# Optimization experiments

Measured on AMD Instinct MI355X. Metric: run time of the kernel, lower is better.

The kernel has to match this reference:

```python
import jax, jax.numpy as jnp
import numpy as np

DIM = 1024
HEADS = 16
HEAD_DIM = DIM // HEADS


def setup_inputs() -> dict:
    key = jax.random.key(0)
    ks = jax.random.split(key, 10)
    B, N, M = 4, 2048, 2048
    s = 1.0 / np.sqrt(DIM)
    return {
        "x": jax.random.normal(ks[0], (B, N, DIM), jnp.float32),
        "context": jax.random.normal(ks[1], (B, M, DIM), jnp.float32),
        "Wq": jax.random.normal(ks[2], (DIM, DIM), jnp.float32) * s,
        "bq": jnp.zeros((DIM,), jnp.float32),
        "Wk": jax.random.normal(ks[3], (DIM, DIM), jnp.float32) * s,
        "bk": jnp.zeros((DIM,), jnp.float32),
        "Wv": jax.random.normal(ks[4], (DIM, DIM), jnp.float32) * s,
        "bv": jnp.zeros((DIM,), jnp.float32),
        "Wo": jax.random.normal(ks[5], (DIM, DIM), jnp.float32) * s,
        "bo": jnp.zeros((DIM,), jnp.float32),
    }


def reference(x, context, Wq, bq, Wk, bk, Wv, bv, Wo, bo):
    B, N, C = x.shape
    M = context.shape[1]
    scale = HEAD_DIM ** (-0.5)
    # projections + split heads: [B, H, L, D]
    q = (x @ Wq.T + bq).reshape(B, N, HEADS, HEAD_DIM).transpose(0, 2, 1, 3)
    k = (context @ Wk.T + bk).reshape(B, M, HEADS, HEAD_DIM).transpose(0, 2, 1, 3)
    v = (context @ Wv.T + bv).reshape(B, M, HEADS, HEAD_DIM).transpose(0, 2, 1, 3)
    attn = jax.nn.softmax(jnp.einsum('bhnd,bhmd->bhnm', q, k) * scale, axis=-1)
    out = jnp.einsum('bhnm,bhmd->bhnd', attn, v)  # [B, H, N, D]
    out = out.transpose(0, 2, 1, 3).reshape(B, N, C)
    return out @ Wo.T + bo
```

## Files before the change

kernel.cpp:

```cpp
#include <hip/hip_runtime.h>
#include <hip/hip_bf16.h>
#include <stdint.h>


#define HEADS 16
#define HD 64
#define NSEQ 2048
#define DIMSZ 1024

typedef __bf16 bf16x8_t __attribute__((ext_vector_type(8)));
typedef float f32x4_t __attribute__((ext_vector_type(4)));
typedef short s16x4 __attribute__((ext_vector_type(4)));
typedef unsigned short u16;
typedef unsigned int u32;

__device__ __forceinline__ u16 f2bf(float f) {
    union { float f; u32 i; } x; x.f = f;
    u32 r = x.i + 0x7FFF + ((x.i >> 16) & 1);
    return (u16)(r >> 16);
}
__device__ __forceinline__ u32 pk2(float a, float b) {
    __hip_bfloat162 h = __float22bfloat162_rn(float2{a, b});
    union { __hip_bfloat162 h2; u32 u; } c; c.h2 = h; return c.u;
}

#if defined(__has_builtin)
#if __has_builtin(__builtin_amdgcn_exp2f)
#define EXP2(x) __builtin_amdgcn_exp2f(x)
#endif
#endif
#ifndef EXP2
#define EXP2(x) exp2f(x)
#endif

__device__ __forceinline__ void pl32swap(u32& a, u32& b) {
    asm("v_permlane32_swap_b32 %0, %1" : "+v"(a), "+v"(b));
}
__device__ __forceinline__ void pl16swap(u32& a, u32& b) {
    asm("v_permlane16_swap_b32 %0, %1" : "+v"(a), "+v"(b));
}

#define GLDS(g, l) __builtin_amdgcn_global_load_lds( \
    (const __attribute__((address_space(1))) void*)(g), \
    (__attribute__((address_space(3))) void*)(l), 16, 0, 0)

__global__ __launch_bounds__(256)
void cvt_all(const float* __restrict__ x, const float* __restrict__ ctx,
             const float* __restrict__ wq, const float* __restrict__ wk,
             const float* __restrict__ wv, const float* __restrict__ wo,
             u16* __restrict__ xb, u16* __restrict__ ctxb,
             u16* __restrict__ wqb, u16* __restrict__ wkb,
             u16* __restrict__ wvb, u16* __restrict__ wob)
{
    long g = (long)blockIdx.x * 256 + threadIdx.x;
    const float* in; u16* out; long off;
    if (g < 1048576L)      { in = x;   out = xb;   off = g; }
    else if (g < 2097152L) { in = ctx; out = ctxb; off = g - 1048576L; }
    else if (g < 2228224L) { in = wq;  out = wqb;  off = g - 2097152L; }
    else if (g < 2359296L) { in = wk;  out = wkb;  off = g - 2228224L; }
    else if (g < 2490368L) { in = wv;  out = wvb;  off = g - 2359296L; }
    else                   { in = wo;  out = wob;  off = g - 2490368L; }
    long i = off * 8;
    float4 a = *(const float4*)(in + i);
    float4 b = *(const float4*)(in + i + 4);
    union { uint4 v; u16 h[8]; } u;
    u.h[0] = f2bf(a.x); u.h[1] = f2bf(a.y); u.h[2] = f2bf(a.z); u.h[3] = f2bf(a.w);
    u.h[4] = f2bf(b.x); u.h[5] = f2bf(b.y); u.h[6] = f2bf(b.z); u.h[7] = f2bf(b.w);
    *(uint4*)(out + i) = u.v;
}

#define BM 128
#define BN 128

#define BKQ 64

__global__ __launch_bounds__(256, 3)
void qkv_gemm(const u16* __restrict__ xb, const u16* __restrict__ ctxb,
              const u16* __restrict__ wq, const u16* __restrict__ wk,
              const u16* __restrict__ wv,
              const float* __restrict__ bq, const float* __restrict__ bk,
              const float* __restrict__ bv,
              u16* __restrict__ qo, u16* __restrict__ ko, u16* __restrict__ vo,
              float qscale)
{
    __shared__ __align__(16) u16 Asm[BM * BKQ];
    __shared__ __align__(16) u16 Wsm[BN * BKQ];

    const int lin  = blockIdx.x + 24 * blockIdx.y;
    const int lin2 = (lin & 7) * 192 + (lin >> 3);
    const int bx   = lin2 % 24;
    const int by   = lin2 / 24;

    const int g    = bx >> 3;
    const int col0 = (bx & 7) * BN;
    const int row0 = by * BM;

    const u16* A = (g == 0) ? xb : ctxb;
    const u16* W = (g == 0) ? wq : (g == 1) ? wk : wv;
    const float* bias = (g == 0) ? bq : (g == 1) ? bk : bv;
    const float scale = (g == 0) ? qscale : 1.0f;

    const int t    = threadIdx.x;
    const int lane = t & 63;
    const int wid  = t >> 6;
    const int lrow = lane & 15;
    const int lq   = lane >> 4;
    const int wm   = (wid >> 1) * 64;
    const int wn   = (wid & 1) * 64;

    const u16* gA[4]; const u16* gW[4];
    u16* lA[4]; u16* lW[4];
    #pragma unroll
    for (int q = 0; q < 4; q++) {
        int s = q * 256 + t;
        int r = s >> 3;
        int c = (s & 7) ^ (r & 7);
        gA[q] = A + (long)(row0 + r) * DIMSZ + c * 8;
        gW[q] = W + (long)(col0 + r) * DIMSZ + c * 8;
        int lofs = (q * 256 + wid * 64) * 8;
        lA[q] = &Asm[lofs];
        lW[q] = &Wsm[lofs];
    }

    f32x4_t zero = {0.f, 0.f, 0.f, 0.f};
    f32x4_t acc[4][4];
    #pragma unroll
    for (int i = 0; i < 4; i++)
        #pragma unroll
        for (int j = 0; j < 4; j++) acc[i][j] = zero;

    const int rsw = lrow & 7;

    if (g < 2) {
        for (int k0 = 0; k0 < DIMSZ; k0 += BKQ) {
            __syncthreads();
            #pragma unroll
            for (int q = 0; q < 4; q++) {
                GLDS(gA[q] + k0, lA[q]);
                GLDS(gW[q] + k0, lW[q]);
            }
            __syncthreads();

            #pragma unroll
            for (int kk = 0; kk < 2; kk++) {
                bf16x8_t af[4], bfr[4];
                #pragma unroll
                for (int i = 0; i < 4; i++)
                    af[i] = *(const bf16x8_t*)
                        &Asm[(wm + 16 * i + lrow) * BKQ + (((kk * 4 + lq) ^ rsw) << 3)];
                #pragma unroll
                for (int j = 0; j < 4; j++)
                    bfr[j] = *(const bf16x8_t*)
                        &Wsm[(wn + 16 * j + lrow) * BKQ + (((kk * 4 + lq) ^ rsw) << 3)];
                #pragma unroll
                for (int i = 0; i < 4; i++)
                    #pragma unroll
                    for (int j = 0; j < 4; j++)
                        acc[i][j] = __builtin_amdgcn_mfma_f32_16x16x32_bf16(
                            bfr[j], af[i], acc[i][j], 0, 0, 0);
            }
        }

        u16* outp = g ? ko : qo;
        #pragma unroll
        for (int j = 0; j < 4; j++) {
            int d0 = col0 + wn + 16 * j + lq * 4;
            f32x4_t bb = *(const f32x4_t*)&bias[d0];
            int h  = d0 >> 6;
            int dl = d0 & 63;
            #pragma unroll
            for (int i = 0; i < 4; i++) {
                int n  = row0 + wm + 16 * i + lrow;
                int b  = n >> 11, nn = n & 2047;
                uint2 p;
                p.x = pk2((acc[i][j][0] + bb[0]) * scale,
                          (acc[i][j][1] + bb[1]) * scale);
                p.y = pk2((acc[i][j][2] + bb[2]) * scale,
                          (acc[i][j][3] + bb[3]) * scale);
                long oidx = ((long)((b * HEADS + h) * NSEQ + nn) << 6) + dl;
                *(uint2*)&outp[oidx] = p;
            }
        }
    } else {
        for (int k0 = 0; k0 < DIMSZ; k0 += BKQ) {
            __syncthreads();
            #pragma unroll
            for (int q = 0; q < 4; q++) {
                GLDS(gA[q] + k0, lA[q]);
                GLDS(gW[q] + k0, lW[q]);
            }
            __syncthreads();

            #pragma unroll
            for (int kk = 0; kk < 2; kk++) {
                bf16x8_t af[4], bfr[4];
                #pragma unroll
                for (int i = 0; i < 4; i++)
                    af[i] = *(const bf16x8_t*)
                        &Asm[(wm + 16 * i + lrow) * BKQ + (((kk * 4 + lq) ^ rsw) << 3)];
                #pragma unroll
                for (int j = 0; j < 4; j++)
                    bfr[j] = *(const bf16x8_t*)
                        &Wsm[(wn + 16 * j + lrow) * BKQ + (((kk * 4 + lq) ^ rsw) << 3)];
                #pragma unroll
                for (int i = 0; i < 4; i++)
                    #pragma unroll
                    for (int j = 0; j < 4; j++)
                        acc[i][j] = __builtin_amdgcn_mfma_f32_16x16x32_bf16(
                            af[i], bfr[j], acc[i][j], 0, 0, 0);
            }
        }

        float bvv[4];
        #pragma unroll
        for (int j = 0; j < 4; j++) bvv[j] = bias[col0 + wn + 16 * j + lrow];

        #pragma unroll
        for (int i = 0; i < 4; i++) {
            int n0 = row0 + wm + 16 * i + lq * 4;
            int b  = n0 >> 11, nn = n0 & 2047;
            #pragma unroll
            for (int j = 0; j < 4; j++) {
                int d = col0 + wn + 16 * j + lrow;
                uint2 p;
                p.x = pk2(acc[i][j][0] + bvv[j], acc[i][j][1] + bvv[j]);
                p.y = pk2(acc[i][j][2] + bvv[j], acc[i][j][3] + bvv[j]);
                long o = ((long)((b * HEADS + (d >> 6)) * HD + (d & 63)) << 11) + nn;
                *(uint2*)&vo[o] = p;
            }
        }
    }
}

#define BKO 64

__global__ __launch_bounds__(256, 2)
void gemm_o(const u16* __restrict__ A, const u16* __restrict__ W,
            const float* __restrict__ bias, float* __restrict__ out)
{
    __shared__ __align__(16) u16 Asm[2][BM * BKO];
    __shared__ __align__(16) u16 Wsm[2][BN * BKO];

    const int lin  = blockIdx.x + 8 * blockIdx.y;
    const int lin2 = (lin & 7) * 64 + (lin >> 3);
    const int col0 = (lin2 & 7) * BN;
    const int row0 = (lin2 >> 3) * BM;

    const int t    = threadIdx.x;
    const int lane = t & 63;
    const int wid  = t >> 6;
    const int lrow = lane & 15;
    const int lq   = lane >> 4;
    const int wm   = (wid >> 1) * 64;
    const int wn   = (wid & 1) * 64;

    const u16* gA[4]; const u16* gW[4]; int lofs[4];
    #pragma unroll
    for (int q = 0; q < 4; q++) {
        int s = q * 256 + t;
        int r = s >> 3;
        int c = (s & 7) ^ (r & 7);
        gA[q] = A + (long)(row0 + r) * DIMSZ + c * 8;
        gW[q] = W + (long)(col0 + r) * DIMSZ + c * 8;
        lofs[q] = (q * 256 + wid * 64) * 8;
    }

    f32x4_t zero = {0.f, 0.f, 0.f, 0.f};
    f32x4_t acc[4][4];
    #pragma unroll
    for (int i = 0; i < 4; i++)
        #pragma unroll
        for (int j = 0; j < 4; j++) acc[i][j] = zero;

    const int rsw = lrow & 7;

    auto stage = [&](int k0, int nb) {
        #pragma unroll
        for (int q = 0; q < 4; q++) {
            GLDS(gA[q] + k0, &Asm[nb][lofs[q]]);
            GLDS(gW[q] + k0, &Wsm[nb][lofs[q]]);
        }
    };
    auto compute = [&](int nb) {
        #pragma unroll
        for (int kk = 0; kk < 2; kk++) {
            bf16x8_t af[4], bfr[4];
            #pragma unroll
            for (int i = 0; i < 4; i++)
                af[i] = *(const bf16x8_t*)
                    &Asm[nb][(wm + 16 * i + lrow) * BKO + (((kk * 4 + lq) ^ rsw) << 3)];
            #pragma unroll
            for (int j = 0; j < 4; j++)
                bfr[j] = *(const bf16x8_t*)
                    &Wsm[nb][(wn + 16 * j + lrow) * BKO + (((kk * 4 + lq) ^ rsw) << 3)];
            #pragma unroll
            for (int i = 0; i < 4; i++)
                #pragma unroll
                for (int j = 0; j < 4; j++)
                    acc[i][j] = __builtin_amdgcn_mfma_f32_16x16x32_bf16(
                        bfr[j], af[i], acc[i][j], 0, 0, 0);
        }
    };

    stage(0, 0);
    __syncthreads();

    for (int k0 = 0; k0 < DIMSZ; k0 += 2 * BKO) {
        stage(k0 + BKO, 1);
        compute(0);
        __syncthreads();
        if (k0 + 2 * BKO < DIMSZ) stage(k0 + 2 * BKO, 0);
        compute(1);
        __syncthreads();
    }

    #pragma unroll
    for (int j = 0; j < 4; j++) {
        int d0 = col0 + wn + 16 * j + lq * 4;
        f32x4_t bb = *(const f32x4_t*)&bias[d0];
        #pragma unroll
        for (int i = 0; i < 4; i++) {
            int n = row0 + wm + 16 * i + lrow;
            f32x4_t v;
            #pragma unroll
            for (int r = 0; r < 4; r++) v[r] = acc[i][j][r] + bb[r];
            *(f32x4_t*)&out[(long)n * DIMSZ + d0] = v;
        }
    }
}

__global__ __launch_bounds__(256, 4)
void attn(const u16* __restrict__ Q, const u16* __restrict__ K,
          const u16* __restrict__ Vt, u16* __restrict__ O)
{
    __shared__ __align__(16) u16 Ksm[2][64 * 64];
    __shared__ __align__(16) u16 Vsm[2][64 * 64];

    const int t    = threadIdx.x;
    const int lane = t & 63;
    const int w    = t >> 6;
    const int lrow = lane & 15;
    const int lq   = lane >> 4;
    const int bh   = blockIdx.x;
    const int q0   = blockIdx.y * 128;
    const int b    = bh >> 4;
    const int h    = bh & 15;

    bf16x8_t qf[2][2];
    #pragma unroll
    for (int qa = 0; qa < 2; qa++) {
        const long qbase = ((long)bh * NSEQ + q0 + w * 32 + qa * 16 + lrow) * HD;
        qf[qa][0] = *(const bf16x8_t*)&Q[qbase + lq * 8];
        qf[qa][1] = *(const bf16x8_t*)&Q[qbase + lq * 8 + 32];
    }

    const long kvbase = (long)bh * NSEQ * HD;

    const u16* gK[2]; const u16* gV[2]; int lofs[2];
    #pragma unroll
    for (int c = 0; c < 2; c++) {
        int s  = c * 256 + t;
        int r  = s >> 3;
        int ch = (s & 7) ^ (r & 7);
        gK[c] = K  + kvbase + (long)r * HD + ch * 8;
        gV[c] = Vt + kvbase + (long)r * NSEQ + ch * 8;
        lofs[c] = (c * 256 + w * 64) * 8;
    }

    f32x4_t zero = {0.f, 0.f, 0.f, 0.f};
    f32x4_t oacc[2][4];
    #pragma unroll
    for (int qa = 0; qa < 2; qa++)
        #pragma unroll
        for (int jd = 0; jd < 4; jd++) oacc[qa][jd] = zero;
    f32x4_t lacc[2] = {zero, zero};

    union { u32 u[4]; bf16x8_t v; } ob;
    ob.u[0] = ob.u[1] = ob.u[2] = ob.u[3] = 0x3F803F80u;
    const bf16x8_t onesb = ob.v;

    const int rsw = lrow & 7;

    auto stage = [&](int ktn, int nb) {
        long ko = (long)ktn * (64 * HD);
        int  vo = ktn * 64;
        GLDS(gK[0] + ko, &Ksm[nb][lofs[0]]);
        GLDS(gK[1] + ko, &Ksm[nb][lofs[1]]);
        GLDS(gV[0] + vo, &Vsm[nb][lofs[0]]);
        GLDS(gV[1] + vo, &Vsm[nb][lofs[1]]);
    };

    auto tile = [&](const u16* Ks, const u16* Vs) {
        #pragma unroll
        for (int t2 = 0; t2 < 2; t2++) {
            f32x4_t sacc[2][2];
            __builtin_amdgcn_s_setprio(1);
            #pragma unroll
            for (int jh = 0; jh < 2; jh++) {
                int jt = t2 * 2 + jh;
                bf16x8_t kf0 = *(const bf16x8_t*)
                    &Ks[(16 * jt + lrow) * 64 + ((lq ^ rsw) << 3)];
                bf16x8_t kf1 = *(const bf16x8_t*)
                    &Ks[(16 * jt + lrow) * 64 + (((4 + lq) ^ rsw) << 3)];
                sacc[jh][0] = __builtin_amdgcn_mfma_f32_16x16x32_bf16(
                    kf0, qf[0][0], zero, 0, 0, 0);
                sacc[jh][1] = __builtin_amdgcn_mfma_f32_16x16x32_bf16(
                    kf0, qf[1][0], zero, 0, 0, 0);
                sacc[jh][0] = __builtin_amdgcn_mfma_f32_16x16x32_bf16(
                    kf1, qf[0][1], sacc[jh][0], 0, 0, 0);
                sacc[jh][1] = __builtin_amdgcn_mfma_f32_16x16x32_bf16(
                    kf1, qf[1][1], sacc[jh][1], 0, 0, 0);
            }
            __builtin_amdgcn_s_setprio(0);

            bf16x8_t pa32[2];
            #pragma unroll
            for (int qa = 0; qa < 2; qa++) {
                u32 uu[2][2];
                #pragma unroll
                for (int jh = 0; jh < 2; jh++) {
                    float p0 = EXP2(sacc[jh][qa][0]);
                    float p1 = EXP2(sacc[jh][qa][1]);
                    float p2 = EXP2(sacc[jh][qa][2]);
                    float p3 = EXP2(sacc[jh][qa][3]);
                    uu[jh][0] = pk2(p0, p1);
                    uu[jh][1] = pk2(p2, p3);
                }
                pl32swap(uu[0][0], uu[1][0]);
                pl16swap(uu[0][0], uu[1][0]);
                pl32swap(uu[0][1], uu[1][1]);
                pl16swap(uu[0][1], uu[1][1]);
                union { u32 u[4]; bf16x8_t v; } pk_;
                pk_.u[0] = uu[0][0]; pk_.u[1] = uu[0][1];
                pk_.u[2] = uu[1][0]; pk_.u[3] = uu[1][1];
                pa32[qa] = pk_.v;
            }

            __builtin_amdgcn_s_setprio(1);
            lacc[0] = __builtin_amdgcn_mfma_f32_16x16x32_bf16(
                pa32[0], onesb, lacc[0], 0, 0, 0);
            lacc[1] = __builtin_amdgcn_mfma_f32_16x16x32_bf16(
                pa32[1], onesb, lacc[1], 0, 0, 0);
            #pragma unroll
            for (int jd = 0; jd < 4; jd++) {
                bf16x8_t vb = *(const bf16x8_t*)
                    &Vs[(16 * jd + lrow) * 64 + (((4 * t2 + lq) ^ rsw) << 3)];
                oacc[0][jd] = __builtin_amdgcn_mfma_f32_16x16x32_bf16(
                    pa32[0], vb, oacc[0][jd], 0, 0, 0);
                oacc[1][jd] = __builtin_amdgcn_mfma_f32_16x16x32_bf16(
                    pa32[1], vb, oacc[1][jd], 0, 0, 0);
            }
            __builtin_amdgcn_s_setprio(0);
        }
    };

    stage(0, 0);
    __syncthreads();

    for (int kt = 0; kt < NSEQ / 64; kt += 2) {
        stage(kt + 1, 1);
        tile(Ksm[0], Vsm[0]);
        __syncthreads();
        if (kt + 2 < NSEQ / 64) stage(kt + 2, 0);
        tile(Ksm[1], Vsm[1]);
        __syncthreads();
    }

    float linv[2][4];
    #pragma unroll
    for (int qa = 0; qa < 2; qa++)
        #pragma unroll
        for (int r = 0; r < 4; r++)
            linv[qa][r] = __builtin_amdgcn_rcpf(lacc[qa][r]);

    #pragma unroll
    for (int qa = 0; qa < 2; qa++) {
        #pragma unroll
        for (int jd = 0; jd < 4; jd++) {
            #pragma unroll
            for (int r = 0; r < 4; r++) {
                int qrow = q0 + w * 32 + qa * 16 + lq * 4 + r;
                int d    = 16 * jd + lrow;
                long oidx = ((long)(b * NSEQ + qrow)) * DIMSZ + h * HD + d;
                O[oidx] = f2bf(oacc[qa][jd][r] * linv[qa][r]);
            }
        }
    }
}

extern "C" void kernel_launch(void* const* d_in, const int* in_sizes, int n_in,
                              void* d_out, int out_size, void* d_ws, size_t ws_size,
                              hipStream_t stream)
{
    const float* x   = (const float*)d_in[0];
    const float* ctx = (const float*)d_in[1];
    const float* Wq  = (const float*)d_in[2];
    const float* bq  = (const float*)d_in[3];
    const float* Wk  = (const float*)d_in[4];
    const float* bk  = (const float*)d_in[5];
    const float* Wv  = (const float*)d_in[6];
    const float* bv  = (const float*)d_in[7];
    const float* Wo  = (const float*)d_in[8];
    const float* bo  = (const float*)d_in[9];
    float* out = (float*)d_out;

    const size_t NX = (size_t)8192 * 1024;
    const size_t NW = (size_t)1024 * 1024;

    u16* xb   = (u16*)d_ws;
    u16* ctxb = xb + NX;
    u16* wqb  = ctxb + NX;
    u16* wkb  = wqb + NW;
    u16* wvb  = wkb + NW;
    u16* wob  = wvb + NW;
    u16* qws  = wob + NW;
    u16* kws  = qws + NX;
    u16* vws  = kws + NX;
    u16* aws  = xb;

    cvt_all<<<10240, 256, 0, stream>>>(x, ctx, Wq, Wk, Wv, Wo,
                                       xb, ctxb, wqb, wkb, wvb, wob);

    const float qscale = 0.125f * 1.44269504088896340736f;

    qkv_gemm<<<dim3(24, 8192 / BM), 256, 0, stream>>>(
        xb, ctxb, wqb, wkb, wvb, bq, bk, bv, qws, kws, vws, qscale);
    attn<<<dim3(64, NSEQ / 128), 256, 0, stream>>>(qws, kws, vws, aws);
    gemm_o<<<dim3(DIMSZ / BN, 8192 / BM), 256, 0, stream>>>(aws, wob, bo, out);
}
```

Baseline: 299.2 us.

## Double-buffer QKV GEMM LDS and enlarge tile to 256x128 with 512 threads

The QKV projection GEMM now uses a 256x128 block tile computed by 8 waves of 512 threads, and double-buffers the LDS tiles. The global-to-LDS load of the next K slice is issued before computing the current one, which removes one barrier per iteration and overlaps memory with MFMA work. The launch becomes a 1D grid of 768 blocks with a remapped swizzle, and the Q/K and V paths share one main loop through a swap flag. LDS use doubles and occupancy targets drop to 2 blocks per CU, which could limit latency hiding.

```diff
diff --git a/kernel.cpp b/kernel.cpp
--- a/kernel.cpp
+++ b/kernel.cpp
@@ -72,9 +72,11 @@
 #define BM 128
 #define BN 128
 
+#define BMQ 256
+#define BNQ 128
 #define BKQ 64
 
-__global__ __launch_bounds__(256, 3)
+__global__ __launch_bounds__(512, 2)
 void qkv_gemm(const u16* __restrict__ xb, const u16* __restrict__ ctxb,
               const u16* __restrict__ wq, const u16* __restrict__ wk,
               const u16* __restrict__ wv,
@@ -83,17 +85,15 @@
               u16* __restrict__ qo, u16* __restrict__ ko, u16* __restrict__ vo,
               float qscale)
 {
-    __shared__ __align__(16) u16 Asm[BM * BKQ];
-    __shared__ __align__(16) u16 Wsm[BN * BKQ];
-
-    const int lin  = blockIdx.x + 24 * blockIdx.y;
-    const int lin2 = (lin & 7) * 192 + (lin >> 3);
-    const int bx   = lin2 % 24;
-    const int by   = lin2 / 24;
-
-    const int g    = bx >> 3;
-    const int col0 = (bx & 7) * BN;
-    const int row0 = by * BM;
+    __shared__ __align__(16) u16 Asm[2][BMQ * BKQ];
+    __shared__ __align__(16) u16 Wsm[2][BNQ * BKQ];
+
+    const int lin  = blockIdx.x;
+    const int lin2 = (lin & 7) * 96 + (lin >> 3);
+    const int g    = lin2 >> 8;
+    const int idx  = lin2 & 255;
+    const int col0 = (idx & 7) * BNQ;
+    const int row0 = (idx >> 3) * BMQ;
 
     const u16* A = (g == 0) ? xb : ctxb;
     const u16* W = (g == 0) ? wq : (g == 1) ? wk : wv;
@@ -108,18 +108,23 @@
     const int wm   = (wid >> 1) * 64;
     const int wn   = (wid & 1) * 64;
 
-    const u16* gA[4]; const u16* gW[4];
-    u16* lA[4]; u16* lW[4];
+    const u16* gA[4]; int lofsA[4];
     #pragma unroll
     for (int q = 0; q < 4; q++) {
-        int s = q * 256 + t;
+        int s = q * 512 + t;
         int r = s >> 3;
         int c = (s & 7) ^ (r & 7);
         gA[q] = A + (long)(row0 + r) * DIMSZ + c * 8;
+        lofsA[q] = (q * 512 + wid * 64) * 8;
+    }
+    const u16* gW[2]; int lofsW[2];
+    #pragma unroll
+    for (int q = 0; q < 2; q++) {
+        int s = q * 512 + t;
+        int r = s >> 3;
+        int c = (s & 7) ^ (r & 7);
         gW[q] = W + (long)(col0 + r) * DIMSZ + c * 8;
-        int lofs = (q * 256 + wid * 64) * 8;
-        lA[q] = &Asm[lofs];
-        lW[q] = &Wsm[lofs];
+        lofsW[q] = (q * 512 + wid * 64) * 8;
     }
 
     f32x4_t zero = {0.f, 0.f, 0.f, 0.f};
@@ -130,37 +135,55 @@
         for (int j = 0; j < 4; j++) acc[i][j] = zero;
 
     const int rsw = lrow & 7;
-
-    if (g < 2) {
-        for (int k0 = 0; k0 < DIMSZ; k0 += BKQ) {
-            __syncthreads();
-            #pragma unroll
-            for (int q = 0; q < 4; q++) {
-                GLDS(gA[q] + k0, lA[q]);
-                GLDS(gW[q] + k0, lW[q]);
-            }
-            __syncthreads();
-
-            #pragma unroll
-            for (int kk = 0; kk < 2; kk++) {
-                bf16x8_t af[4], bfr[4];
-                #pragma unroll
-                for (int i = 0; i < 4; i++)
-                    af[i] = *(const bf16x8_t*)
-                        &Asm[(wm + 16 * i + lrow) * BKQ + (((kk * 4 + lq) ^ rsw) << 3)];
-                #pragma unroll
-                for (int j = 0; j < 4; j++)
-                    bfr[j] = *(const bf16x8_t*)
-                        &Wsm[(wn + 16 * j + lrow) * BKQ + (((kk * 4 + lq) ^ rsw) << 3)];
+    const bool swap = (g < 2);
+
+    auto stage = [&](int k0, int nb) {
+        #pragma unroll
+        for (int q = 0; q < 4; q++) GLDS(gA[q] + k0, &Asm[nb][lofsA[q]]);
+        #pragma unroll
+        for (int q = 0; q < 2; q++) GLDS(gW[q] + k0, &Wsm[nb][lofsW[q]]);
+    };
+    auto compute = [&](int nb) {
+        #pragma unroll
+        for (int kk = 0; kk < 2; kk++) {
+            bf16x8_t af[4], bfr[4];
+            #pragma unroll
+            for (int i = 0; i < 4; i++)
+                af[i] = *(const bf16x8_t*)
+                    &Asm[nb][(wm + 16 * i + lrow) * BKQ + (((kk * 4 + lq) ^ rsw) << 3)];
+            #pragma unroll
+            for (int j = 0; j < 4; j++)
+                bfr[j] = *(const bf16x8_t*)
+                    &Wsm[nb][(wn + 16 * j + lrow) * BKQ + (((kk * 4 + lq) ^ rsw) << 3)];
+            if (swap) {
                 #pragma unroll
                 for (int i = 0; i < 4; i++)
                     #pragma unroll
                     for (int j = 0; j < 4; j++)
                         acc[i][j] = __builtin_amdgcn_mfma_f32_16x16x32_bf16(
                             bfr[j], af[i], acc[i][j], 0, 0, 0);
-            }
-        }
-
+            } else {
+                #pragma unroll
+                for (int i = 0; i < 4; i++)
+                    #pragma unroll
+                    for (int j = 0; j < 4; j++)
+                        acc[i][j] = __builtin_amdgcn_mfma_f32_16x16x32_bf16(
+                            af[i], bfr[j], acc[i][j], 0, 0, 0);
+            }
+        }
+    };
+
+    stage(0, 0);
+    __syncthreads();
+    int nb = 0;
+    for (int k0 = 0; k0 < DIMSZ; k0 += BKQ) {
+        if (k0 + BKQ < DIMSZ) stage(k0 + BKQ, nb ^ 1);
+        compute(nb);
+        __syncthreads();
+        nb ^= 1;
+    }
+
+    if (g < 2) {
         u16* outp = g ? ko : qo;
         #pragma unroll
         for (int j = 0; j < 4; j++) {
@@ -182,35 +205,6 @@
             }
         }
     } else {
-        for (int k0 = 0; k0 < DIMSZ; k0 += BKQ) {
-            __syncthreads();
-            #pragma unroll
-            for (int q = 0; q < 4; q++) {
-                GLDS(gA[q] + k0, lA[q]);
-                GLDS(gW[q] + k0, lW[q]);
-            }
-            __syncthreads();
-
-            #pragma unroll
-            for (int kk = 0; kk < 2; kk++) {
-                bf16x8_t af[4], bfr[4];
-                #pragma unroll
-                for (int i = 0; i < 4; i++)
-                    af[i] = *(const bf16x8_t*)
-                        &Asm[(wm + 16 * i + lrow) * BKQ + (((kk * 4 + lq) ^ rsw) << 3)];
-                #pragma unroll
-                for (int j = 0; j < 4; j++)
-                    bfr[j] = *(const bf16x8_t*)
-                        &Wsm[(wn + 16 * j + lrow) * BKQ + (((kk * 4 + lq) ^ rsw) << 3)];
-                #pragma unroll
-                for (int i = 0; i < 4; i++)
-                    #pragma unroll
-                    for (int j = 0; j < 4; j++)
-                        acc[i][j] = __builtin_amdgcn_mfma_f32_16x16x32_bf16(
-                            af[i], bfr[j], acc[i][j], 0, 0, 0);
-            }
-        }
-
         float bvv[4];
         #pragma unroll
         for (int j = 0; j < 4; j++) bvv[j] = bias[col0 + wn + 16 * j + lrow];
@@ -523,7 +517,7 @@
 
     const float qscale = 0.125f * 1.44269504088896340736f;
 
-    qkv_gemm<<<dim3(24, 8192 / BM), 256, 0, stream>>>(
+    qkv_gemm<<<768, 512, 0, stream>>>(
         xb, ctxb, wqb, wkb, wvb, bq, bk, bv, qws, kws, vws, qscale);
     attn<<<dim3(64, NSEQ / 128), 256, 0, stream>>>(qws, kws, vws, aws);
     gemm_o<<<dim3(DIMSZ / BN, 8192 / BM), 256, 0, stream>>>(aws, wob, bo, out);
```

Result: slower. 312.0 us (+4.3%).
